# Optimization experiments

Hardware: AMD Instinct MI355X
Metric: run time of the kernel (lower is better)

The kernel has to match this reference:

```python
import jax, jax.numpy as jnp
import numpy as np

EPS = 1e-5


def _corr_matrix(A):
    # A: [n, f]. Standardize each column with unbiased std (torch.std default,
    # ddof=1), then all-pairs correlation as a single GEMM, matching
    # mean(x_std * y_std) over the batch dim for every column pair.
    n = A.shape[0]
    mu = A.mean(axis=0, keepdims=True)
    sd = A.std(axis=0, ddof=1, keepdims=True)
    As = (A - mu) / (sd + EPS)            # [n, f]
    return (As.T @ As) / n                 # [f, f]


def setup_inputs() -> dict:
    key = jax.random.key(0)
    kx, ky = jax.random.split(key)
    X = jax.random.normal(kx, (8192, 1024), dtype=jnp.float32)
    Y = jax.random.normal(ky, (8192, 1024), dtype=jnp.float32)
    return {"X": X, "Y": Y}


def reference(X, Y):
    f = X.shape[1]
    diff = _corr_matrix(X) - _corr_matrix(Y)          # [f, f]
    mask = jnp.triu(jnp.ones((f, f), dtype=diff.dtype), k=1)  # pairs i<j
    count = f * (f - 1) // 2
    loss = jnp.sum((diff * diff) * mask) / count
    return loss
```

## Files before the change

### kernel.cpp

```cpp
#include <hip/hip_runtime.h>
#include <hip/hip_bf16.h>
#include <stdint.h>

#define NROWS 8192
#define NF    1024
#define EPSV  1e-5f

typedef __attribute__((ext_vector_type(8))) short bf16x8;
typedef __attribute__((ext_vector_type(4))) float f32x4;

static __device__ __forceinline__ unsigned short f2bf(float v) {
    __hip_bfloat16 b = __float2bfloat16(v);
    return *reinterpret_cast<unsigned short*>(&b);
}
static __device__ __forceinline__ float bf2f(unsigned short u) {
    union { uint32_t i; float f; } cv; cv.i = (uint32_t)u << 16; return cv.f;
}

__global__ void transpose_stats(const float* __restrict__ X, const float* __restrict__ Y,
                                unsigned short* __restrict__ Xst, unsigned short* __restrict__ Yst,
                                float* __restrict__ psum, float* __restrict__ psq) {
    __shared__ unsigned short sbuf[64][68];
    int ct  = blockIdx.x;
    int rt  = blockIdx.y;
    int mat = blockIdx.z;
    const float* A = mat ? Y : X;
    unsigned short* O = mat ? Yst : Xst;
    int tid = threadIdx.x;
    #pragma unroll
    for (int it = 0; it < 4; ++it) {
        int idx = it * 256 + tid;
        int row = idx >> 4;
        int c4  = idx & 15;
        float4 v = *reinterpret_cast<const float4*>(
            A + (size_t)(rt * 64 + row) * NF + ct * 64 + c4 * 4);
        ushort4 o;
        o.x = f2bf(v.x); o.y = f2bf(v.y); o.z = f2bf(v.z); o.w = f2bf(v.w);
        *reinterpret_cast<ushort4*>(&sbuf[row][c4 * 4]) = o;
    }
    __syncthreads();
    {
        int c  = tid >> 2;
        int r8 = tid & 3;
        bf16x8 v0, v1;
        float s = 0.f, sq = 0.f;
        #pragma unroll
        for (int i = 0; i < 8; ++i) {
            unsigned short u = sbuf[r8 * 16 + i][c];
            v0[i] = (short)u;
            float f = bf2f(u); s += f; sq += f * f;
        }
        #pragma unroll
        for (int i = 0; i < 8; ++i) {
            unsigned short u = sbuf[r8 * 16 + 8 + i][c];
            v1[i] = (short)u;
            float f = bf2f(u); s += f; sq += f * f;
        }
        unsigned short* dst = O + (size_t)(ct * 64 + c) * NROWS + rt * 64 + r8 * 16;
        *reinterpret_cast<bf16x8*>(dst)     = v0;
        *reinterpret_cast<bf16x8*>(dst + 8) = v1;
        s  += __shfl_xor(s, 1);  s  += __shfl_xor(s, 2);
        sq += __shfl_xor(sq, 1); sq += __shfl_xor(sq, 2);
        if (r8 == 0) {
            int pidx = (mat * 128 + rt) * NF + ct * 64 + c;
            psum[pidx] = s;
            psq[pidx]  = sq;
        }
    }
}

__global__ void stats_final(const float* __restrict__ psum, const float* __restrict__ psq,
                            float* __restrict__ mu, float* __restrict__ isd) {
    __shared__ float ls[4][64], lq[4][64];
    int mat  = blockIdx.y;
    int col0 = blockIdx.x * 64;
    int colq = threadIdx.x & 63;
    int g    = threadIdx.x >> 6;
    int col  = col0 + colq;
    float s = 0.f, sq = 0.f;
    #pragma unroll
    for (int k = 0; k < 32; ++k) {
        int idx = (mat * 128 + g * 32 + k) * NF + col;
        s  += psum[idx];
        sq += psq[idx];
    }
    ls[g][colq] = s; lq[g][colq] = sq;
    __syncthreads();
    if (g == 0) {
        s  = ls[0][colq] + ls[1][colq] + ls[2][colq] + ls[3][colq];
        sq = lq[0][colq] + lq[1][colq] + lq[2][colq] + lq[3][colq];
        float m   = s / (float)NROWS;
        float var = (sq - s * m) / (float)(NROWS - 1);
        var = fmaxf(var, 0.f);
        mu [mat * NF + col] = m;
        isd[mat * NF + col] = 1.0f / (sqrtf(var) + EPSV);
    }
}

__global__ __launch_bounds__(256, 2) void gram_fused(
    const unsigned short* __restrict__ Xst, const unsigned short* __restrict__ Yst,
    const float* __restrict__ mu, const float* __restrict__ isd,
    unsigned short* __restrict__ Cdiff, int nsplit, int kper) {
    __shared__ short lds[8][128 * 32];
    int nwg = 36 * nsplit, cpx = nwg >> 3;
    int bid = blockIdx.x;
    int swz = (bid & 7) * cpx + (bid >> 3);
    int split = swz / 36, tile = swz % 36;
    int r = 0, t0 = tile;
    while (t0 >= 8 - r) { t0 -= 8 - r; ++r; }
    int c = r + t0;
    const short* Xs = reinterpret_cast<const short*>(Xst);
    const short* Ys = reinterpret_cast<const short*>(Yst);
    int tid = threadIdx.x, lane = tid & 63, wid = tid >> 6;
    int wr = wid >> 1, wc = wid & 1;
    f32x4 accX[4][4] = {}, accY[4][4] = {};
    int k0 = split * kper;
    int nstep = kper >> 5;
    int s8 = ((lane & 3) - (lane >> 3)) & 3;

    auto stage = [&](const short* M, short* bA, short* bB, int ts) {
        int kk = k0 + ts * 32;
        #pragma unroll
        for (int i = 0; i < 2; ++i) {
            int chunk = wid * 2 + i;
            int rw = chunk * 16 + (lane >> 2);
            size_t ko = (size_t)kk + s8 * 8;
            const short* ga = M + (size_t)(r * 128 + rw) * NROWS + ko;
            __builtin_amdgcn_global_load_lds(
                (const __attribute__((address_space(1))) void*)ga,
                (__attribute__((address_space(3))) void*)(bA + chunk * 512), 16, 0, 0);
            const short* gb = M + (size_t)(c * 128 + rw) * NROWS + ko;
            __builtin_amdgcn_global_load_lds(
                (const __attribute__((address_space(1))) void*)gb,
                (__attribute__((address_space(3))) void*)(bB + chunk * 512), 16, 0, 0);
        }
    };
    auto compute = [&](const short* bA, const short* bB, f32x4 (&acc)[4][4]) {
        bf16x8 a[4], b[4];
        int rl = lane & 15;
        int sl = ((lane >> 4) + (rl >> 1)) & 3;
        #pragma unroll
        for (int f = 0; f < 4; ++f) {
            a[f] = *reinterpret_cast<const bf16x8*>(bA + (wr * 64 + f * 16 + rl) * 32 + sl * 8);
            b[f] = *reinterpret_cast<const bf16x8*>(bB + (wc * 64 + f * 16 + rl) * 32 + sl * 8);
        }
        __builtin_amdgcn_s_setprio(1);
        #pragma unroll
        for (int fm = 0; fm < 4; ++fm)
            #pragma unroll
            for (int fn = 0; fn < 4; ++fn)
                acc[fm][fn] = __builtin_amdgcn_mfma_f32_16x16x32_bf16(
                    a[fm], b[fn], acc[fm][fn], 0, 0, 0);
        __builtin_amdgcn_s_setprio(0);
    };

    stage(Xs, lds[0], lds[2], 0);
    stage(Ys, lds[4], lds[6], 0);
    for (int t = 0; t < nstep; ++t) {
        int cur = t & 1, nxt = cur ^ 1;
        int tn = (t + 1) & (nstep - 1);
        stage(Xs, lds[0 + nxt], lds[2 + nxt], tn);
        asm volatile("s_waitcnt vmcnt(8)" ::: "memory");
        __builtin_amdgcn_s_barrier();
        __builtin_amdgcn_sched_barrier(0);
        compute(lds[0 + cur], lds[2 + cur], accX);
        stage(Ys, lds[4 + nxt], lds[6 + nxt], tn);
        asm volatile("s_waitcnt vmcnt(8)" ::: "memory");
        __builtin_amdgcn_s_barrier();
        __builtin_amdgcn_sched_barrier(0);
        compute(lds[4 + cur], lds[6 + cur], accY);
    }
    asm volatile("s_waitcnt vmcnt(0)" ::: "memory");

    const float* mux = mu;        const float* muy = mu  + NF;
    const float* isx = isd;       const float* isy = isd + NF;
    const float inv_n = 1.0f / (float)NROWS;
    float f0 = (split == 0) ? 1.0f : 0.0f;
    float mxc[4], ixc[4], myc[4], iyc[4];
    #pragma unroll
    for (int fn = 0; fn < 4; ++fn) {
        int cf = c * 128 + wc * 64 + fn * 16 + (lane & 15);
        mxc[fn] = mux[cf]; ixc[fn] = isx[cf];
        myc[fn] = muy[cf]; iyc[fn] = isy[cf];
    }
    unsigned short* Cp = Cdiff + ((size_t)split * 36 + tile) * 16384;
    #pragma unroll
    for (int fm = 0; fm < 4; ++fm)
        #pragma unroll
        for (int reg = 0; reg < 4; ++reg) {
            int rf = r * 128 + wr * 64 + fm * 16 + (lane >> 4) * 4 + reg;
            float mxr = mux[rf], ixr = isx[rf];
            float myr = muy[rf], iyr = isy[rf];
            int rowl = wr * 64 + fm * 16 + (lane >> 4) * 4 + reg;
            #pragma unroll
            for (int fn = 0; fn < 4; ++fn) {
                float cx = (accX[fm][fn][reg] * inv_n - f0 * mxr * mxc[fn]) * ixr * ixc[fn];
                float cy = (accY[fm][fn][reg] * inv_n - f0 * myr * myc[fn]) * iyr * iyc[fn];
                int coll = wc * 64 + fn * 16 + (lane & 15);
                Cp[rowl * 128 + coll] = f2bf(cx - cy);
            }
        }
}

__global__ void reduce_loss(const unsigned short* __restrict__ Cdiff, float* __restrict__ out,
                            int nsplit) {
    int tile = blockIdx.x, sub = blockIdx.y;
    int r = 0, t = tile;
    while (t >= 8 - r) { t -= 8 - r; ++r; }
    int c = r + t;
    float s = 0.f;
    for (int e4 = threadIdx.x; e4 < 512; e4 += 256) {
        int row  = sub * 16 + (e4 >> 5);
        int col0 = (e4 & 31) * 4;
        float d0 = 0.f, d1 = 0.f, d2 = 0.f, d3 = 0.f;
        for (int sp = 0; sp < nsplit; ++sp) {
            ushort4 v = *reinterpret_cast<const ushort4*>(
                Cdiff + ((size_t)sp * 36 + tile) * 16384 + row * 128 + col0);
            d0 += bf2f(v.x); d1 += bf2f(v.y); d2 += bf2f(v.z); d3 += bf2f(v.w);
        }
        float dv[4] = {d0, d1, d2, d3};
        #pragma unroll
        for (int j = 0; j < 4; ++j) {
            int col = col0 + j;
            if (r == c && col <= row) continue;
            s += dv[j] * dv[j];
        }
    }
    #pragma unroll
    for (int off = 32; off > 0; off >>= 1) s += __shfl_down(s, off, 64);
    __shared__ float wsum[4];
    int lane = threadIdx.x & 63, wid = threadIdx.x >> 6;
    if (lane == 0) wsum[wid] = s;
    __syncthreads();
    if (threadIdx.x == 0) {
        float tot = wsum[0] + wsum[1] + wsum[2] + wsum[3];
        atomicAdd(out, tot * (1.0f / 523776.0f));
    }
}

extern "C" void kernel_launch(void* const* d_in, const int* in_sizes, int n_in,
                              void* d_out, int out_size, void* d_ws, size_t ws_size,
                              hipStream_t stream) {
    const float* X = (const float*)d_in[0];
    const float* Y = (const float*)d_in[1];
    char* ws = (char*)d_ws;

    auto need = [](int ns) -> size_t {
        return ((size_t)32 << 20)
             + (size_t)ns * 36 * 16384 * 2
             + (size_t)2 * 128 * NF * 4 * 2
             + (size_t)2 * NF * 4 * 2;
    };
    int nsplit = 16;
    if (ws_size < need(16)) nsplit = 8;
    if (ws_size < need(8))  nsplit = 4;
    int kper = NROWS / nsplit;

    unsigned short* Xst = (unsigned short*)(ws);
    unsigned short* Yst = (unsigned short*)(ws + ((size_t)16 << 20));
    unsigned short* Cdiff = (unsigned short*)(ws + ((size_t)32 << 20));
    size_t cd_sz = (size_t)nsplit * 36 * 16384 * 2;
    float* psum = (float*)(ws + ((size_t)32 << 20) + cd_sz);
    float* psq  = psum + 2 * 128 * NF;
    float* mu   = psq  + 2 * 128 * NF;
    float* isd  = mu   + 2 * NF;
    float* out  = (float*)d_out;

    hipMemsetAsync(out, 0, sizeof(float), stream);
    transpose_stats<<<dim3(16, 128, 2), 256, 0, stream>>>(X, Y, Xst, Yst, psum, psq);
    stats_final<<<dim3(16, 2), 256, 0, stream>>>(psum, psq, mu, isd);
    gram_fused<<<36 * nsplit, 256, 0, stream>>>(Xst, Yst, mu, isd, Cdiff, nsplit, kper);
    reduce_loss<<<dim3(36, 8), 256, 0, stream>>>(Cdiff, out, nsplit);
}
```

Baseline: 163.6 us.

## Switch gram kernel to a 3-slot interleaved X/Y LDS ring for higher occupancy

The gram kernel replaces its double-buffered X and Y LDS staging (8 tiles) with a single 3-slot ring (6 tiles) that alternates X and Y k-steps. Each step now has one wait and one barrier. With less LDS per workgroup, launch bounds rise from 2 to 3 workgroups per CU, aiming to hide memory latency with more resident waves and fewer barriers. Tradeoffs: register pressure is tighter under the new launch bound. Also, a slot is refilled with no barrier after other waves' last read of it, which could create a write-after-read race.

```diff
diff --git a/kernel.cpp b/kernel.cpp
--- a/kernel.cpp
+++ b/kernel.cpp
@@ -97,11 +97,11 @@
     }
 }
 
-__global__ __launch_bounds__(256, 2) void gram_fused(
+__global__ __launch_bounds__(256, 3) void gram_fused(
     const unsigned short* __restrict__ Xst, const unsigned short* __restrict__ Yst,
     const float* __restrict__ mu, const float* __restrict__ isd,
     unsigned short* __restrict__ Cdiff, int nsplit, int kper) {
-    __shared__ short lds[8][128 * 32];
+    __shared__ short lds[6][128 * 32];
     int nwg = 36 * nsplit, cpx = nwg >> 3;
     int bid = blockIdx.x;
     int swz = (bid & 7) * cpx + (bid >> 3);
@@ -116,10 +116,16 @@
     f32x4 accX[4][4] = {}, accY[4][4] = {};
     int k0 = split * kper;
     int nstep = kper >> 5;
+    int P = nstep * 2;
     int s8 = ((lane & 3) - (lane >> 3)) & 3;
 
-    auto stage = [&](const short* M, short* bA, short* bB, int ts) {
-        int kk = k0 + ts * 32;
+    auto pstage = [&](int q) {
+        int qq = (q < P) ? q : (q - P);
+        const short* M = (qq & 1) ? Ys : Xs;
+        int slot = q % 3;
+        short* bA = lds[2 * slot];
+        short* bB = lds[2 * slot + 1];
+        int kk = k0 + (qq >> 1) * 32;
         #pragma unroll
         for (int i = 0; i < 2; ++i) {
             int chunk = wid * 2 + i;
@@ -135,7 +141,9 @@
                 (__attribute__((address_space(3))) void*)(bB + chunk * 512), 16, 0, 0);
         }
     };
-    auto compute = [&](const short* bA, const short* bB, f32x4 (&acc)[4][4]) {
+    auto compute = [&](int slot, f32x4 (&acc)[4][4]) {
+        const short* bA = lds[2 * slot];
+        const short* bB = lds[2 * slot + 1];
         bf16x8 a[4], b[4];
         int rl = lane & 15;
         int sl = ((lane >> 4) + (rl >> 1)) & 3;
@@ -154,21 +162,15 @@
         __builtin_amdgcn_s_setprio(0);
     };
 
-    stage(Xs, lds[0], lds[2], 0);
-    stage(Ys, lds[4], lds[6], 0);
-    for (int t = 0; t < nstep; ++t) {
-        int cur = t & 1, nxt = cur ^ 1;
-        int tn = (t + 1) & (nstep - 1);
-        stage(Xs, lds[0 + nxt], lds[2 + nxt], tn);
+    pstage(0);
+    pstage(1);
+    for (int p = 0; p < P; ++p) {
+        pstage(p + 2);
         asm volatile("s_waitcnt vmcnt(8)" ::: "memory");
         __builtin_amdgcn_s_barrier();
         __builtin_amdgcn_sched_barrier(0);
-        compute(lds[0 + cur], lds[2 + cur], accX);
-        stage(Ys, lds[4 + nxt], lds[6 + nxt], tn);
-        asm volatile("s_waitcnt vmcnt(8)" ::: "memory");
-        __builtin_amdgcn_s_barrier();
-        __builtin_amdgcn_sched_barrier(0);
-        compute(lds[4 + cur], lds[6 + cur], accY);
+        if (p & 1) compute(p % 3, accY);
+        else       compute(p % 3, accX);
     }
     asm volatile("s_waitcnt vmcnt(0)" ::: "memory");
 
```

After: 367.6 us. 125% more time.

## Load MFMA operands directly from global memory instead of LDS staging

Applied to the files above, without the earlier changes.

Drops the LDS double-buffered staging (global_load_lds plus barriers) in the Gram kernel. Each wave now loads its bf16x8 MFMA fragments straight from global memory into registers every k-step. This removes LDS traffic and the workgroup barriers. In exchange it loses data sharing between waves, so global/L2 reads rise, and it loses explicit prefetch pipelining, which exposes load latency.

```diff
diff --git a/kernel.cpp b/kernel.cpp
--- a/kernel.cpp
+++ b/kernel.cpp
@@ -101,7 +101,6 @@
     const unsigned short* __restrict__ Xst, const unsigned short* __restrict__ Yst,
     const float* __restrict__ mu, const float* __restrict__ isd,
     unsigned short* __restrict__ Cdiff, int nsplit, int kper) {
-    __shared__ short lds[8][128 * 32];
     int nwg = 36 * nsplit, cpx = nwg >> 3;
     int bid = blockIdx.x;
     int swz = (bid & 7) * cpx + (bid >> 3);
@@ -113,64 +112,41 @@
     const short* Ys = reinterpret_cast<const short*>(Yst);
     int tid = threadIdx.x, lane = tid & 63, wid = tid >> 6;
     int wr = wid >> 1, wc = wid & 1;
+    int rl = lane & 15, kq = lane >> 4;
     f32x4 accX[4][4] = {}, accY[4][4] = {};
     int k0 = split * kper;
+
+    int baseA[4], baseB[4];
+    #pragma unroll
+    for (int f = 0; f < 4; ++f) {
+        baseA[f] = (r * 128 + wr * 64 + f * 16 + rl) * NROWS + k0 + kq * 8;
+        baseB[f] = (c * 128 + wc * 64 + f * 16 + rl) * NROWS + k0 + kq * 8;
+    }
+
     int nstep = kper >> 5;
-    int s8 = ((lane & 3) - (lane >> 3)) & 3;
-
-    auto stage = [&](const short* M, short* bA, short* bB, int ts) {
-        int kk = k0 + ts * 32;
-        #pragma unroll
-        for (int i = 0; i < 2; ++i) {
-            int chunk = wid * 2 + i;
-            int rw = chunk * 16 + (lane >> 2);
-            size_t ko = (size_t)kk + s8 * 8;
-            const short* ga = M + (size_t)(r * 128 + rw) * NROWS + ko;
-            __builtin_amdgcn_global_load_lds(
-                (const __attribute__((address_space(1))) void*)ga,
-                (__attribute__((address_space(3))) void*)(bA + chunk * 512), 16, 0, 0);
-            const short* gb = M + (size_t)(c * 128 + rw) * NROWS + ko;
-            __builtin_amdgcn_global_load_lds(
-                (const __attribute__((address_space(1))) void*)gb,
-                (__attribute__((address_space(3))) void*)(bB + chunk * 512), 16, 0, 0);
-        }
-    };
-    auto compute = [&](const short* bA, const short* bB, f32x4 (&acc)[4][4]) {
-        bf16x8 a[4], b[4];
-        int rl = lane & 15;
-        int sl = ((lane >> 4) + (rl >> 1)) & 3;
+    for (int t = 0; t < nstep; ++t) {
+        int kk = t * 32;
+        bf16x8 ax[4], bx[4], ay[4], by[4];
         #pragma unroll
         for (int f = 0; f < 4; ++f) {
-            a[f] = *reinterpret_cast<const bf16x8*>(bA + (wr * 64 + f * 16 + rl) * 32 + sl * 8);
-            b[f] = *reinterpret_cast<const bf16x8*>(bB + (wc * 64 + f * 16 + rl) * 32 + sl * 8);
-        }
-        __builtin_amdgcn_s_setprio(1);
+            ax[f] = *reinterpret_cast<const bf16x8*>(Xs + baseA[f] + kk);
+            bx[f] = *reinterpret_cast<const bf16x8*>(Xs + baseB[f] + kk);
+            ay[f] = *reinterpret_cast<const bf16x8*>(Ys + baseA[f] + kk);
+            by[f] = *reinterpret_cast<const bf16x8*>(Ys + baseB[f] + kk);
+        }
         #pragma unroll
         for (int fm = 0; fm < 4; ++fm)
             #pragma unroll
             for (int fn = 0; fn < 4; ++fn)
-                acc[fm][fn] = __builtin_amdgcn_mfma_f32_16x16x32_bf16(
-                    a[fm], b[fn], acc[fm][fn], 0, 0, 0);
-        __builtin_amdgcn_s_setprio(0);
-    };
-
-    stage(Xs, lds[0], lds[2], 0);
-    stage(Ys, lds[4], lds[6], 0);
-    for (int t = 0; t < nstep; ++t) {
-        int cur = t & 1, nxt = cur ^ 1;
-        int tn = (t + 1) & (nstep - 1);
-        stage(Xs, lds[0 + nxt], lds[2 + nxt], tn);
-        asm volatile("s_waitcnt vmcnt(8)" ::: "memory");
-        __builtin_amdgcn_s_barrier();
-        __builtin_amdgcn_sched_barrier(0);
-        compute(lds[0 + cur], lds[2 + cur], accX);
-        stage(Ys, lds[4 + nxt], lds[6 + nxt], tn);
-        asm volatile("s_waitcnt vmcnt(8)" ::: "memory");
-        __builtin_amdgcn_s_barrier();
-        __builtin_amdgcn_sched_barrier(0);
-        compute(lds[4 + cur], lds[6 + cur], accY);
-    }
-    asm volatile("s_waitcnt vmcnt(0)" ::: "memory");
+                accX[fm][fn] = __builtin_amdgcn_mfma_f32_16x16x32_bf16(
+                    ax[fm], bx[fn], accX[fm][fn], 0, 0, 0);
+        #pragma unroll
+        for (int fm = 0; fm < 4; ++fm)
+            #pragma unroll
+            for (int fn = 0; fn < 4; ++fn)
+                accY[fm][fn] = __builtin_amdgcn_mfma_f32_16x16x32_bf16(
+                    ay[fm], by[fn], accY[fm][fn], 0, 0, 0);
+    }
 
     const float* mux = mu;        const float* muy = mu  + NF;
     const float* isx = isd;       const float* isy = isd + NF;
```

Result: slower. 249.1 us (+52.3%).

## Split X and Y Gram computation into separate workgroups with single-buffered LDS

Applied to the files above, without the earlier changes.

The fused Gram kernel, which computed both X and Y correlation tiles in one workgroup, is replaced by a kernel that handles one matrix per workgroup. This doubles the grid and halves accumulator registers and LDS use, raising the occupancy target from 2 to 3 waves per SIMD. The software-pipelined double-buffered loads are dropped in favour of a plain sync-load-sync-compute loop. The difference X-Y now happens in the reduction kernel, which costs twice the partial-result writes and reads plus workspace, and the lost load/compute overlap may expose memory latency.

```diff
diff --git a/kernel.cpp b/kernel.cpp
--- a/kernel.cpp
+++ b/kernel.cpp
@@ -97,29 +97,32 @@
     }
 }
 
-__global__ __launch_bounds__(256, 2) void gram_fused(
+__global__ __launch_bounds__(256, 3) void gram_part(
     const unsigned short* __restrict__ Xst, const unsigned short* __restrict__ Yst,
     const float* __restrict__ mu, const float* __restrict__ isd,
-    unsigned short* __restrict__ Cdiff, int nsplit, int kper) {
-    __shared__ short lds[8][128 * 32];
-    int nwg = 36 * nsplit, cpx = nwg >> 3;
+    unsigned short* __restrict__ Cpart, int nsplit, int kper) {
+    __shared__ short As[128 * 32];
+    __shared__ short Bs[128 * 32];
+    int nwg = 72 * nsplit, cpx = nwg >> 3;
     int bid = blockIdx.x;
     int swz = (bid & 7) * cpx + (bid >> 3);
-    int split = swz / 36, tile = swz % 36;
+    int mat = swz / (36 * nsplit);
+    int rem = swz % (36 * nsplit);
+    int split = rem / 36, tile = rem % 36;
     int r = 0, t0 = tile;
     while (t0 >= 8 - r) { t0 -= 8 - r; ++r; }
     int c = r + t0;
-    const short* Xs = reinterpret_cast<const short*>(Xst);
-    const short* Ys = reinterpret_cast<const short*>(Yst);
+    const short* M = reinterpret_cast<const short*>(mat ? Yst : Xst);
     int tid = threadIdx.x, lane = tid & 63, wid = tid >> 6;
     int wr = wid >> 1, wc = wid & 1;
-    f32x4 accX[4][4] = {}, accY[4][4] = {};
+    f32x4 acc[4][4] = {};
     int k0 = split * kper;
     int nstep = kper >> 5;
     int s8 = ((lane & 3) - (lane >> 3)) & 3;
 
-    auto stage = [&](const short* M, short* bA, short* bB, int ts) {
-        int kk = k0 + ts * 32;
+    for (int t = 0; t < nstep; ++t) {
+        int kk = k0 + t * 32;
+        __syncthreads();
         #pragma unroll
         for (int i = 0; i < 2; ++i) {
             int chunk = wid * 2 + i;
@@ -128,21 +131,20 @@
             const short* ga = M + (size_t)(r * 128 + rw) * NROWS + ko;
             __builtin_amdgcn_global_load_lds(
                 (const __attribute__((address_space(1))) void*)ga,
-                (__attribute__((address_space(3))) void*)(bA + chunk * 512), 16, 0, 0);
+                (__attribute__((address_space(3))) void*)(As + chunk * 512), 16, 0, 0);
             const short* gb = M + (size_t)(c * 128 + rw) * NROWS + ko;
             __builtin_amdgcn_global_load_lds(
                 (const __attribute__((address_space(1))) void*)gb,
-                (__attribute__((address_space(3))) void*)(bB + chunk * 512), 16, 0, 0);
-        }
-    };
-    auto compute = [&](const short* bA, const short* bB, f32x4 (&acc)[4][4]) {
+                (__attribute__((address_space(3))) void*)(Bs + chunk * 512), 16, 0, 0);
+        }
+        __syncthreads();
         bf16x8 a[4], b[4];
         int rl = lane & 15;
         int sl = ((lane >> 4) + (rl >> 1)) & 3;
         #pragma unroll
         for (int f = 0; f < 4; ++f) {
-            a[f] = *reinterpret_cast<const bf16x8*>(bA + (wr * 64 + f * 16 + rl) * 32 + sl * 8);
-            b[f] = *reinterpret_cast<const bf16x8*>(bB + (wc * 64 + f * 16 + rl) * 32 + sl * 8);
+            a[f] = *reinterpret_cast<const bf16x8*>(As + (wr * 64 + f * 16 + rl) * 32 + sl * 8);
+            b[f] = *reinterpret_cast<const bf16x8*>(Bs + (wc * 64 + f * 16 + rl) * 32 + sl * 8);
         }
         __builtin_amdgcn_s_setprio(1);
         #pragma unroll
@@ -152,57 +154,36 @@
                 acc[fm][fn] = __builtin_amdgcn_mfma_f32_16x16x32_bf16(
                     a[fm], b[fn], acc[fm][fn], 0, 0, 0);
         __builtin_amdgcn_s_setprio(0);
-    };
-
-    stage(Xs, lds[0], lds[2], 0);
-    stage(Ys, lds[4], lds[6], 0);
-    for (int t = 0; t < nstep; ++t) {
-        int cur = t & 1, nxt = cur ^ 1;
-        int tn = (t + 1) & (nstep - 1);
-        stage(Xs, lds[0 + nxt], lds[2 + nxt], tn);
-        asm volatile("s_waitcnt vmcnt(8)" ::: "memory");
-        __builtin_amdgcn_s_barrier();
-        __builtin_amdgcn_sched_barrier(0);
-        compute(lds[0 + cur], lds[2 + cur], accX);
-        stage(Ys, lds[4 + nxt], lds[6 + nxt], tn);
-        asm volatile("s_waitcnt vmcnt(8)" ::: "memory");
-        __builtin_amdgcn_s_barrier();
-        __builtin_amdgcn_sched_barrier(0);
-        compute(lds[4 + cur], lds[6 + cur], accY);
-    }
-    asm volatile("s_waitcnt vmcnt(0)" ::: "memory");
-
-    const float* mux = mu;        const float* muy = mu  + NF;
-    const float* isx = isd;       const float* isy = isd + NF;
+    }
+
+    const float* mum = mu  + mat * NF;
+    const float* ism = isd + mat * NF;
     const float inv_n = 1.0f / (float)NROWS;
     float f0 = (split == 0) ? 1.0f : 0.0f;
-    float mxc[4], ixc[4], myc[4], iyc[4];
+    float mc[4], ic[4];
     #pragma unroll
     for (int fn = 0; fn < 4; ++fn) {
         int cf = c * 128 + wc * 64 + fn * 16 + (lane & 15);
-        mxc[fn] = mux[cf]; ixc[fn] = isx[cf];
-        myc[fn] = muy[cf]; iyc[fn] = isy[cf];
-    }
-    unsigned short* Cp = Cdiff + ((size_t)split * 36 + tile) * 16384;
+        mc[fn] = mum[cf]; ic[fn] = ism[cf];
+    }
+    unsigned short* Cp = Cpart + ((size_t)(mat * nsplit + split) * 36 + tile) * 16384;
     #pragma unroll
     for (int fm = 0; fm < 4; ++fm)
         #pragma unroll
         for (int reg = 0; reg < 4; ++reg) {
             int rf = r * 128 + wr * 64 + fm * 16 + (lane >> 4) * 4 + reg;
-            float mxr = mux[rf], ixr = isx[rf];
-            float myr = muy[rf], iyr = isy[rf];
+            float mr = mum[rf], ir = ism[rf];
             int rowl = wr * 64 + fm * 16 + (lane >> 4) * 4 + reg;
             #pragma unroll
             for (int fn = 0; fn < 4; ++fn) {
-                float cx = (accX[fm][fn][reg] * inv_n - f0 * mxr * mxc[fn]) * ixr * ixc[fn];
-                float cy = (accY[fm][fn][reg] * inv_n - f0 * myr * myc[fn]) * iyr * iyc[fn];
+                float cx = (acc[fm][fn][reg] * inv_n - f0 * mr * mc[fn]) * ir * ic[fn];
                 int coll = wc * 64 + fn * 16 + (lane & 15);
-                Cp[rowl * 128 + coll] = f2bf(cx - cy);
+                Cp[rowl * 128 + coll] = f2bf(cx);
             }
         }
 }
 
-__global__ void reduce_loss(const unsigned short* __restrict__ Cdiff, float* __restrict__ out,
+__global__ void reduce_loss(const unsigned short* __restrict__ Cpart, float* __restrict__ out,
                             int nsplit) {
     int tile = blockIdx.x, sub = blockIdx.y;
     int r = 0, t = tile;
@@ -214,9 +195,14 @@
         int col0 = (e4 & 31) * 4;
         float d0 = 0.f, d1 = 0.f, d2 = 0.f, d3 = 0.f;
         for (int sp = 0; sp < nsplit; ++sp) {
-            ushort4 v = *reinterpret_cast<const ushort4*>(
-                Cdiff + ((size_t)sp * 36 + tile) * 16384 + row * 128 + col0);
-            d0 += bf2f(v.x); d1 += bf2f(v.y); d2 += bf2f(v.z); d3 += bf2f(v.w);
+            ushort4 vx = *reinterpret_cast<const ushort4*>(
+                Cpart + ((size_t)sp * 36 + tile) * 16384 + row * 128 + col0);
+            ushort4 vy = *reinterpret_cast<const ushort4*>(
+                Cpart + ((size_t)(nsplit + sp) * 36 + tile) * 16384 + row * 128 + col0);
+            d0 += bf2f(vx.x) - bf2f(vy.x);
+            d1 += bf2f(vx.y) - bf2f(vy.y);
+            d2 += bf2f(vx.z) - bf2f(vy.z);
+            d3 += bf2f(vx.w) - bf2f(vy.w);
         }
         float dv[4] = {d0, d1, d2, d3};
         #pragma unroll
@@ -247,7 +233,7 @@
 
     auto need = [](int ns) -> size_t {
         return ((size_t)32 << 20)
-             + (size_t)ns * 36 * 16384 * 2
+             + (size_t)2 * ns * 36 * 16384 * 2
              + (size_t)2 * 128 * NF * 4 * 2
              + (size_t)2 * NF * 4 * 2;
     };
@@ -258,9 +244,9 @@
 
     unsigned short* Xst = (unsigned short*)(ws);
     unsigned short* Yst = (unsigned short*)(ws + ((size_t)16 << 20));
-    unsigned short* Cdiff = (unsigned short*)(ws + ((size_t)32 << 20));
-    size_t cd_sz = (size_t)nsplit * 36 * 16384 * 2;
-    float* psum = (float*)(ws + ((size_t)32 << 20) + cd_sz);
+    unsigned short* Cpart = (unsigned short*)(ws + ((size_t)32 << 20));
+    size_t cp_sz = (size_t)2 * nsplit * 36 * 16384 * 2;
+    float* psum = (float*)(ws + ((size_t)32 << 20) + cp_sz);
     float* psq  = psum + 2 * 128 * NF;
     float* mu   = psq  + 2 * 128 * NF;
     float* isd  = mu   + 2 * NF;
@@ -269,6 +255,6 @@
     hipMemsetAsync(out, 0, sizeof(float), stream);
     transpose_stats<<<dim3(16, 128, 2), 256, 0, stream>>>(X, Y, Xst, Yst, psum, psq);
     stats_final<<<dim3(16, 2), 256, 0, stream>>>(psum, psq, mu, isd);
-    gram_fused<<<36 * nsplit, 256, 0, stream>>>(Xst, Yst, mu, isd, Cdiff, nsplit, kper);
-    reduce_loss<<<dim3(36, 8), 256, 0, stream>>>(Cdiff, out, nsplit);
-}
+    gram_part<<<72 * nsplit, 256, 0, stream>>>(Xst, Yst, mu, isd, Cpart, nsplit, kper);
+    reduce_loss<<<dim3(36, 8), 256, 0, stream>>>(Cpart, out, nsplit);
+}
```

Result: no change. 164.3 us (+0.4%).
